# Kernel optimization log

Measured on AMD Instinct MI355X. Metric: run time of the kernel, lower is better.

The kernel has to match this reference:

```python
import jax, jax.numpy as jnp
import numpy as np
import math

B, S, D, H = 16, 1024, 1024, 16
HD = D // H  # head_dim = 64

def setup_inputs() -> dict:
    key = jax.random.key(0)
    ks = jax.random.split(key, 10)
    def lin_w(k, out_d, in_d):
        bound = 1.0 / math.sqrt(in_d)
        return jax.random.uniform(k, (out_d, in_d), jnp.float32, -bound, bound)
    return {
        "x": jax.random.normal(ks[0], (B, S, D), jnp.float32),
        "attention_mask_indices": jnp.ones((B, S, 1), dtype=bool),
        "wq_w": lin_w(ks[1], D, D), "wq_b": jnp.zeros((D,), jnp.float32),
        "wk_w": lin_w(ks[2], D, D), "wk_b": jnp.zeros((D,), jnp.float32),
        "wv_w": lin_w(ks[3], D, D), "wv_b": jnp.zeros((D,), jnp.float32),
        "wo_w": lin_w(ks[4], D, D), "wo_b": jnp.zeros((D,), jnp.float32),
    }

def reference(x, attention_mask_indices, wq_w, wq_b, wk_w, wk_b, wv_w, wv_b, wo_w, wo_b):
    bsz, seqlen, _ = x.shape
    # torch Linear: y = x @ W^T + b
    xq = (x @ wq_w.T + wq_b).reshape(bsz, seqlen, H, HD)
    xk = (x @ wk_w.T + wk_b).reshape(bsz, seqlen, H, HD)
    xv = (x @ wv_w.T + wv_b).reshape(bsz, seqlen, H, HD)
    # n_kv_heads == n_heads -> repeat_kv is identity
    scores = jnp.einsum("bqhd,bkhd->bhqk", xq, xk) / math.sqrt(HD)
    mask = attention_mask_indices[:, None, None, :, 0]  # [b,1,1,s]
    scores = jnp.where(mask, scores, jnp.finfo(scores.dtype).min)
    probs = jax.nn.softmax(scores.astype(jnp.float32), axis=-1)
    out = jnp.einsum("bhqk,bkhd->bqhd", probs, xv).reshape(bsz, seqlen, D)
    return out @ wo_w.T + wo_b
```

## Files before the change

kernel.cpp:

```cpp
#include <hip/hip_runtime.h>
#include <hip/hip_bf16.h>

typedef __bf16 bf16;
typedef bf16  bf16x4 __attribute__((ext_vector_type(4)));
typedef bf16  bf16x8 __attribute__((ext_vector_type(8)));
typedef float f32x4  __attribute__((ext_vector_type(4)));

#define B_  16
#define S_  1024
#define D_  1024
#define H_  16
#define HD_ 64

typedef __attribute__((address_space(3))) void lds_void_t;
typedef __attribute__((address_space(1))) void g_void_t;
__device__ __forceinline__ void gl_lds16(const void* g, void* l) {
    __builtin_amdgcn_global_load_lds(
        (const g_void_t*)(uintptr_t)g,
        (lds_void_t*)(uint32_t)(uintptr_t)l, 16, 0, 0);
}

#define BARRIER()     asm volatile("s_barrier" ::: "memory")
#define WAIT_LGKM(n)  do { asm volatile("s_waitcnt lgkmcnt(" #n ")" ::: "memory"); \
                           __builtin_amdgcn_sched_barrier(0); } while (0)
#define WAIT_VM(n)    asm volatile("s_waitcnt vmcnt(" #n ")" ::: "memory")
#define SCHED_PIN()   __builtin_amdgcn_sched_barrier(0)
#define PRIO1()       __builtin_amdgcn_s_setprio(1)
#define PRIO0()       __builtin_amdgcn_s_setprio(0)

__global__ __launch_bounds__(256) void cvt_f32_bf16(
    const float* __restrict__ s, bf16* __restrict__ d, int n)
{
    int i = (blockIdx.x * 256 + threadIdx.x) * 8;
    if (i >= n) return;
    f32x4 a = *(const f32x4*)(s + i);
    f32x4 b = *(const f32x4*)(s + i + 4);
    bf16x8 r;
    for (int j = 0; j < 4; j++) { r[j] = (bf16)a[j]; r[4 + j] = (bf16)b[j]; }
    *(bf16x8*)(d + i) = r;
}

template <bool QKV, int NBY, typename TC>
__global__ __launch_bounds__(512, 2) void gemm8(
    const bf16* __restrict__ A, const bf16* __restrict__ Bw,
    const float* __restrict__ b0, const float* __restrict__ b1,
    const float* __restrict__ b2,
    TC* __restrict__ C, int ldc,
    bf16* __restrict__ Qd, bf16* __restrict__ Kd, bf16* __restrict__ Vd)
{
    __shared__ char lds[131072];

    const int tid  = threadIdx.x;
    const int w    = tid >> 6;
    const int lane = tid & 63;
    const int l15  = lane & 15;
    const int quad = lane >> 4;
    const int wm   = w >> 2;
    const int wn   = w & 3;

    const int nwg = gridDim.x;
    const int lin = blockIdx.x;
    const int swz = (lin & 7) * (nwg >> 3) + (lin >> 3);
    const int bx  = swz / NBY;
    const int by  = swz - bx * NBY;
    const int m0  = bx * 256;
    const int n0  = by * 256;

    const int rl0 = w * 16 + (lane >> 3);
    const int rl1 = rl0 + 8;
    const int sc  = (((lane & 7) ^ ((lane >> 3) & 7))) * 16;
    char* const ld0 = (char*)lds + w * 2048;

    const char* aS0; const char* aS1;
    int bidx = 0, m0loc = 0;
    if constexpr (QKV) {
        aS0 = (const char*)A + (size_t)(m0 + rl0) * 2048 + sc;
        aS1 = (const char*)A + (size_t)(m0 + rl1) * 2048 + sc;
    } else {
        bidx  = m0 >> 10; m0loc = m0 & 1023;
        aS0 = (const char*)A + ((size_t)bidx * 16 * 1024 + m0loc + rl0) * 128 + sc;
        aS1 = (const char*)A + ((size_t)bidx * 16 * 1024 + m0loc + rl1) * 128 + sc;
    }
    const char* bS0 = (const char*)Bw + (size_t)(n0 + rl0) * 2048 + sc;
    const char* bS1 = (const char*)Bw + (size_t)(n0 + rl1) * 2048 + sc;

    auto stageA = [&](int slot, int t, int half) {
        size_t go;
        if constexpr (QKV) go = (size_t)half * 262144 + (size_t)t * 128;
        else               go = (size_t)t * 131072 + (size_t)half * 16384;
        gl_lds16(aS0 + go, ld0 + slot * 16384);
        gl_lds16(aS1 + go, ld0 + slot * 16384 + 1024);
    };
    auto stageB = [&](int slot, int t, int half) {
        size_t go = (size_t)half * 262144 + (size_t)t * 128;
        gl_lds16(bS0 + go, ld0 + slot * 16384);
        gl_lds16(bS1 + go, ld0 + slot * 16384 + 1024);
    };

    const int cx0 = ((quad    ) ^ (l15 & 7)) * 16;
    const int cx1 = ((quad | 4) ^ (l15 & 7)) * 16;
    const char* aEv0 = (char*)lds + wm * 16384 + l15 * 128 + cx0;
    const char* aEv1 = (char*)lds + wm * 16384 + l15 * 128 + cx1;
    const char* bEv0 = (char*)lds + 32768 + (wn >> 1) * 16384 + (wn & 1) * 8192
                       + l15 * 128 + cx0;
    const char* bEv1 = (char*)lds + 32768 + (wn >> 1) * 16384 + (wn & 1) * 8192
                       + l15 * 128 + cx1;
    const char* aOd0 = aEv0 + 65536;
    const char* aOd1 = aEv1 + 65536;
    const char* bOd0 = bEv0 + 65536;
    const char* bOd1 = bEv1 + 65536;

    bf16x8 a03[4][2], a47[4][2], bE[4][2], bO[4][2];
    f32x4 acc[8][4];
    #pragma unroll
    for (int i = 0; i < 8; i++)
        #pragma unroll
        for (int j = 0; j < 4; j++)
            acc[i][j] = (f32x4){0.f, 0.f, 0.f, 0.f};

    auto rdA = [&](bf16x8 (&dst)[4][2], const char* p0, const char* p1, int ro) {
        #pragma unroll
        for (int mf = 0; mf < 4; mf++) {
            dst[mf][0] = *(const bf16x8*)(p0 + (ro + mf) * 2048);
            dst[mf][1] = *(const bf16x8*)(p1 + (ro + mf) * 2048);
        }
    };
    auto rdB2 = [&](bf16x8 (&dst)[4][2], int lo, const char* p0, const char* p1) {
        #pragma unroll
        for (int nf = 0; nf < 2; nf++) {
            dst[lo + nf][0] = *(const bf16x8*)(p0 + (lo + nf) * 2048);
            dst[lo + nf][1] = *(const bf16x8*)(p1 + (lo + nf) * 2048);
        }
    };
    auto mfq = [&](bf16x8 (&af)[4][2], bf16x8 (&bf_)[4][2], int nlo, int mlo) {
        #pragma unroll
        for (int mf = 0; mf < 4; mf++)
            #pragma unroll
            for (int nf = 0; nf < 2; nf++) {
                f32x4 c = acc[mlo + mf][nlo + nf];
                c = __builtin_amdgcn_mfma_f32_16x16x32_bf16(
                        af[mf][0], bf_[nlo + nf][0], c, 0, 0, 0);
                c = __builtin_amdgcn_mfma_f32_16x16x32_bf16(
                        af[mf][1], bf_[nlo + nf][1], c, 0, 0, 0);
                acc[mlo + mf][nlo + nf] = c;
            }
    };

    stageA(0, 0, 0); stageA(1, 0, 1); stageB(2, 0, 0); stageB(3, 0, 1);
    stageB(6, 1, 0); stageB(7, 1, 1);
    stageA(4, 1, 0); stageA(5, 1, 1);
    WAIT_VM(8);
    BARRIER();
    rdA(a03, aEv0, aEv1, 0);

    for (int i = 0; i < 8; ++i) {
        const int t2 = (2 * i + 2) & 15, t3 = (2 * i + 3) & 15;
        rdB2(bE, 0, bEv0, bEv1);
        WAIT_LGKM(0); PRIO1(); mfq(a03, bE, 0, 0); PRIO0(); BARRIER();
        rdB2(bE, 2, bEv0, bEv1);
        SCHED_PIN();
        rdA(a47, aEv0, aEv1, 4);
        WAIT_LGKM(8); PRIO1(); mfq(a03, bE, 2, 0); PRIO0();
        WAIT_VM(0); BARRIER();
        rdA(a03, aOd0, aOd1, 0);
        stageB(2, t2, 0); stageB(3, t2, 1);
        WAIT_LGKM(8); PRIO1(); mfq(a47, bE, 0, 4); PRIO0(); BARRIER();
        rdB2(bO, 0, bOd0, bOd1);
        stageA(0, t2, 0); stageA(1, t2, 1);
        WAIT_LGKM(8); PRIO1(); mfq(a47, bE, 2, 4); PRIO0(); BARRIER();
        rdB2(bO, 2, bOd0, bOd1);
        SCHED_PIN();
        rdA(a47, aOd0, aOd1, 4);
        WAIT_LGKM(8); PRIO1(); mfq(a03, bO, 0, 0); PRIO0(); BARRIER();
        stageB(6, t3, 0);
        WAIT_LGKM(8); PRIO1(); mfq(a03, bO, 2, 0); PRIO0();
        WAIT_VM(2); BARRIER();
        rdA(a03, aEv0, aEv1, 0);
        stageB(7, t3, 1);
        WAIT_LGKM(8); PRIO1(); mfq(a47, bO, 0, 4); PRIO0(); BARRIER();
        stageA(4, t3, 0); stageA(5, t3, 1);
        WAIT_LGKM(8); PRIO1(); mfq(a47, bO, 2, 4); PRIO0();
        WAIT_VM(4); BARRIER();
    }

    if constexpr (QKV) {
        const int seg = n0 >> 10;
        const int cb  = n0 & 1023;
        const float* bp = seg == 0 ? b0 : (seg == 1 ? b1 : b2);
        if (seg < 2) {
            bf16* dst = (seg == 0) ? Qd : Kd;
            #pragma unroll
            for (int mf = 0; mf < 8; mf++)
                #pragma unroll
                for (int nf = 0; nf < 4; nf++) {
                    int col = cb + wn * 64 + nf * 16 + l15;
                    int hh = col >> 6, dd = col & 63;
                    float bb = bp[col];
                    #pragma unroll
                    for (int r = 0; r < 4; r++) {
                        int row = m0 + wm * 128 + mf * 16 + quad * 4 + r;
                        int bl = row >> 10, s = row & 1023;
                        dst[((size_t)(bl * 16 + hh) * 1024 + s) * 64 + dd] =
                            (bf16)(acc[mf][nf][r] + bb);
                    }
                }
        } else {
            #pragma unroll
            for (int mf = 0; mf < 8; mf++)
                #pragma unroll
                for (int nf = 0; nf < 4; nf++) {
                    int col = cb + wn * 64 + nf * 16 + l15;
                    int hh = col >> 6, dd = col & 63;
                    float bb = bp[col];
                    int row0 = m0 + wm * 128 + mf * 16 + quad * 4;
                    int bl = row0 >> 10, s0 = row0 & 1023;
                    bf16x4 pk;
                    #pragma unroll
                    for (int r = 0; r < 4; r++) pk[r] = (bf16)(acc[mf][nf][r] + bb);
                    *(bf16x4*)&Vd[(((size_t)(bl * 16 + hh) * 16 + (s0 >> 6)) * 64 + dd) * 64
                                  + (s0 & 63)] = pk;
                }
        }
    } else {
        #pragma unroll
        for (int mf = 0; mf < 8; mf++)
            #pragma unroll
            for (int nf = 0; nf < 4; nf++) {
                int col = n0 + wn * 64 + nf * 16 + l15;
                float bb = b0[col];
                #pragma unroll
                for (int r = 0; r < 4; r++) {
                    int row = m0 + wm * 128 + mf * 16 + quad * 4 + r;
                    C[(size_t)row * ldc + col] = (TC)(acc[mf][nf][r] + bb);
                }
            }
    }
}

__global__ __launch_bounds__(256) void attn_fused(
    bf16* __restrict__ Qh, const bf16* __restrict__ Kh,
    const bf16* __restrict__ Vt)
{
    const int qt = blockIdx.x, h = blockIdx.y, b = blockIdx.z;
    const int tid  = threadIdx.x;
    const int w    = tid >> 6;
    const int lane = tid & 63;
    const int l15  = lane & 15;
    const int quad = lane >> 4;

    __shared__ bf16 lds[36864];
    bf16* Pw = lds + 18432 + w * 4608;

    const int nIss = (w == 0) ? 3 : 2;
    int gofs[3];
    for (int j = 0; j < nIss; j++) {
        int c = (w + j * 4) * 64 + lane;
        int row = c / 9;
        int o = c - row * 9;
        if (o == 8) o = 0;
        gofs[j] = (row * 8 + o) * 16;
    }

    const float qscale = 0.125f * 1.44269504088896f;
    bf16* Qbase = Qh + ((size_t)(b * 16 + h) * 1024 + qt * 256 + w * 64) * 64;
    bf16x8 aq[4][2];
    for (int mt = 0; mt < 4; mt++)
        for (int c = 0; c < 2; c++) {
            bf16x8 v = *(const bf16x8*)&Qbase[(mt * 16 + l15) * 64 + c * 32 + quad * 8];
            for (int j = 0; j < 8; j++) v[j] = (bf16)((float)v[j] * qscale);
            aq[mt][c] = v;
        }

    bf16x8 ones;
    for (int j = 0; j < 8; j++) ones[j] = (bf16)1.0f;

    f32x4 acc[4][4], accL[4];
    for (int i = 0; i < 4; i++) {
        accL[i] = (f32x4){0.f, 0.f, 0.f, 0.f};
        for (int j = 0; j < 4; j++) acc[i][j] = (f32x4){0.f, 0.f, 0.f, 0.f};
    }

    const bf16* Ktb = Kh + (size_t)(b * 16 + h) * 65536;
    const bf16* Vtb = Vt + (size_t)(b * 16 + h) * 65536;

    auto stage = [&](int kt, int cur) {
        const char* Ktile = (const char*)(Ktb + kt * 4096);
        const char* Vtile = (const char*)(Vtb + kt * 4096);
        char* Kd = (char*)lds + cur * 18432;
        for (int j = 0; j < nIss; j++) {
            int is = w + j * 4;
            gl_lds16(Ktile + gofs[j], Kd + is * 1024);
            gl_lds16(Vtile + gofs[j], Kd + 9216 + is * 1024);
        }
    };

    stage(0, 0);

    for (int kt = 0; kt < 16; kt++) {
        const int cur = kt & 1;
        if (kt < 15) {
            stage(kt + 1, cur ^ 1);
            if (w == 0) { WAIT_VM(6); } else { WAIT_VM(4); }
        } else {
            WAIT_VM(0);
        }
        BARRIER();

        const bf16* Ks = lds + cur * 9216;
        const bf16* Vs = Ks + 4608;

        bf16x8 bk[4][2];
        for (int nt = 0; nt < 4; nt++)
            for (int c = 0; c < 2; c++)
                bk[nt][c] = *(const bf16x8*)&Ks[(nt * 16 + l15) * 72 + c * 32 + quad * 8];

        f32x4 sf[4][4];
        for (int nt = 0; nt < 4; nt++)
            for (int mt = 0; mt < 4; mt++) {
                f32x4 z = (f32x4){0.f, 0.f, 0.f, 0.f};
                z = __builtin_amdgcn_mfma_f32_16x16x32_bf16(bk[nt][0], aq[mt][0], z, 0, 0, 0);
                sf[nt][mt] = __builtin_amdgcn_mfma_f32_16x16x32_bf16(bk[nt][1], aq[mt][1], z, 0, 0, 0);
            }

        for (int mt = 0; mt < 4; mt++)
            for (int nt = 0; nt < 4; nt++) {
                bf16x4 pk;
                for (int r = 0; r < 4; r++)
                    pk[r] = (bf16)__builtin_amdgcn_exp2f(sf[nt][mt][r]);
                *(bf16x4*)&Pw[(mt * 16 + l15) * 72 + nt * 16 + quad * 4] = pk;
            }

        WAIT_LGKM(0);

        bf16x8 pa[4][2];
        for (int mt = 0; mt < 4; mt++)
            for (int c = 0; c < 2; c++)
                pa[mt][c] = *(const bf16x8*)&Pw[(mt * 16 + l15) * 72 + c * 32 + quad * 8];
        for (int mt = 0; mt < 4; mt++) {
            accL[mt] = __builtin_amdgcn_mfma_f32_16x16x32_bf16(pa[mt][0], ones, accL[mt], 0, 0, 0);
            accL[mt] = __builtin_amdgcn_mfma_f32_16x16x32_bf16(pa[mt][1], ones, accL[mt], 0, 0, 0);
        }
        bf16x8 bv[4][2];
        for (int nt = 0; nt < 4; nt++)
            for (int c = 0; c < 2; c++)
                bv[nt][c] = *(const bf16x8*)&Vs[(nt * 16 + l15) * 72 + c * 32 + quad * 8];
        for (int mt = 0; mt < 4; mt++)
            for (int nt = 0; nt < 4; nt++) {
                acc[mt][nt] = __builtin_amdgcn_mfma_f32_16x16x32_bf16(pa[mt][0], bv[nt][0], acc[mt][nt], 0, 0, 0);
                acc[mt][nt] = __builtin_amdgcn_mfma_f32_16x16x32_bf16(pa[mt][1], bv[nt][1], acc[mt][nt], 0, 0, 0);
            }
        BARRIER();
    }

    for (int mt = 0; mt < 4; mt++)
        for (int r = 0; r < 4; r++) {
            float rl = 1.f / accL[mt][r];
            for (int nt = 0; nt < 4; nt++)
                Qbase[(mt * 16 + quad * 4 + r) * 64 + nt * 16 + l15] =
                    (bf16)(acc[mt][nt][r] * rl);
        }
}

extern "C" void kernel_launch(void* const* d_in, const int* in_sizes, int n_in,
                              void* d_out, int out_size, void* d_ws, size_t ws_size,
                              hipStream_t stream)
{
    const float* x    = (const float*)d_in[0];
    const float* wq_w = (const float*)d_in[2];
    const float* wq_b = (const float*)d_in[3];
    const float* wk_w = (const float*)d_in[4];
    const float* wk_b = (const float*)d_in[5];
    const float* wv_w = (const float*)d_in[6];
    const float* wv_b = (const float*)d_in[7];
    const float* wo_w = (const float*)d_in[8];
    const float* wo_b = (const float*)d_in[9];
    float* out = (float*)d_out;

    const size_t MEL = 1024 * 1024;
    int CH = 16;
    if (ws_size != 0)
        while (CH > 1 && (4 + 4 * (size_t)CH) * MEL * sizeof(bf16) > ws_size) CH >>= 1;

    bf16* wqkvb = (bf16*)d_ws;
    bf16* wob   = wqkvb + 3 * MEL;
    bf16* xb    = wob + MEL;
    bf16* Qh    = xb + (size_t)CH * MEL;
    bf16* Kh    = Qh + (size_t)CH * MEL;
    bf16* Vtb   = Kh + (size_t)CH * MEL;

    dim3 blk(256);
    cvt_f32_bf16<<<512, blk, 0, stream>>>(wq_w, wqkvb,           (int)MEL);
    cvt_f32_bf16<<<512, blk, 0, stream>>>(wk_w, wqkvb + MEL,     (int)MEL);
    cvt_f32_bf16<<<512, blk, 0, stream>>>(wv_w, wqkvb + 2 * MEL, (int)MEL);
    cvt_f32_bf16<<<512, blk, 0, stream>>>(wo_w, wob,             (int)MEL);

    for (int c0 = 0; c0 < B_; c0 += CH) {
        const int Mc = CH * S_;
        cvt_f32_bf16<<<Mc * 1024 / 2048, blk, 0, stream>>>(
            x + (size_t)c0 * S_ * D_, xb, Mc * 1024);

        gemm8<true, 12, bf16><<<dim3((Mc / 256) * 12), dim3(512), 0, stream>>>(
            xb, wqkvb, wq_b, wk_b, wv_b,
            (bf16*)nullptr, 0, Qh, Kh, Vtb);

        attn_fused<<<dim3(4, H_, CH), blk, 0, stream>>>(Qh, Kh, Vtb);

        gemm8<false, 4, float><<<dim3((Mc / 256) * 4), dim3(512), 0, stream>>>(
            Qh, wob, wo_b, nullptr, nullptr,
            out + (size_t)c0 * S_ * D_, 1024, nullptr, nullptr, nullptr);
    }
}
```

Before: 396.1 us.

## Pass attention probabilities through registers via bpermute and drop P LDS buffer

Replaces the per-wave LDS round trip for the softmax probability tile with ds_bpermute lane shuffles that rearrange the S-MFMA output into the A-operand layout for the PV MFMA. The row sum moves from extra MFMAs against a ones vector to scalar accumulation plus cross-lane shuffles at the end. This halves the shared memory footprint, sets launch bounds to ask for 3 blocks per CU, and remaps block indices so neighbouring blocks are spread across batch-heads. The aim is fewer LDS writes and reads, less MFMA work and higher occupancy, at the cost of more VALU and bpermute traffic and possible register pressure.

```diff
diff --git a/kernel.cpp b/kernel.cpp
--- a/kernel.cpp
+++ b/kernel.cpp
@@ -237,19 +237,22 @@
     }
 }
 
-__global__ __launch_bounds__(256) void attn_fused(
+__global__ __launch_bounds__(256, 3) void attn_fused(
     bf16* __restrict__ Qh, const bf16* __restrict__ Kh,
     const bf16* __restrict__ Vt)
 {
-    const int qt = blockIdx.x, h = blockIdx.y, b = blockIdx.z;
     const int tid  = threadIdx.x;
     const int w    = tid >> 6;
     const int lane = tid & 63;
     const int l15  = lane & 15;
     const int quad = lane >> 4;
 
-    __shared__ bf16 lds[36864];
-    bf16* Pw = lds + 18432 + w * 4608;
+    const int lin = blockIdx.x + (blockIdx.y << 2) + (blockIdx.z << 6);
+    const int ppx = (int)gridDim.z * 2;
+    const int bh  = (lin & 7) * ppx + ((lin >> 3) >> 2);
+    const int qt  = (lin >> 3) & 3;
+
+    __shared__ bf16 lds[18432];
 
     const int nIss = (w == 0) ? 3 : 2;
     int gofs[3];
@@ -262,26 +265,27 @@
     }
 
     const float qscale = 0.125f * 1.44269504088896f;
-    bf16* Qbase = Qh + ((size_t)(b * 16 + h) * 1024 + qt * 256 + w * 64) * 64;
+    bf16* Qbase = Qh + ((size_t)bh * 1024 + qt * 256 + w * 64) * 64;
     bf16x8 aq[4][2];
+    #pragma unroll
     for (int mt = 0; mt < 4; mt++)
+        #pragma unroll
         for (int c = 0; c < 2; c++) {
             bf16x8 v = *(const bf16x8*)&Qbase[(mt * 16 + l15) * 64 + c * 32 + quad * 8];
+            #pragma unroll
             for (int j = 0; j < 8; j++) v[j] = (bf16)((float)v[j] * qscale);
             aq[mt][c] = v;
         }
 
-    bf16x8 ones;
-    for (int j = 0; j < 8; j++) ones[j] = (bf16)1.0f;
-
-    f32x4 acc[4][4], accL[4];
-    for (int i = 0; i < 4; i++) {
-        accL[i] = (f32x4){0.f, 0.f, 0.f, 0.f};
+    f32x4 acc[4][4];
+    float lsum[4] = {0.f, 0.f, 0.f, 0.f};
+    #pragma unroll
+    for (int i = 0; i < 4; i++)
+        #pragma unroll
         for (int j = 0; j < 4; j++) acc[i][j] = (f32x4){0.f, 0.f, 0.f, 0.f};
-    }
-
-    const bf16* Ktb = Kh + (size_t)(b * 16 + h) * 65536;
-    const bf16* Vtb = Vt + (size_t)(b * 16 + h) * 65536;
+
+    const bf16* Ktb = Kh + (size_t)bh * 65536;
+    const bf16* Vtb = Vt + (size_t)bh * 65536;
 
     auto stage = [&](int kt, int cur) {
         const char* Ktile = (const char*)(Ktb + kt * 4096);
@@ -294,6 +298,11 @@
         }
     };
 
+    const bool qe = ((quad & 1) == 0);
+    const bool ql = (quad < 2);
+    const int  a1 = (l15 + 16 * (((quad & 1) << 1) | (quad >> 1))) << 2;
+    const int  a2 = a1 ^ 64;
+
     stage(0, 0);
 
     for (int kt = 0; kt < 16; kt++) {
@@ -309,52 +318,82 @@
         const bf16* Ks = lds + cur * 9216;
         const bf16* Vs = Ks + 4608;
 
-        bf16x8 bk[4][2];
-        for (int nt = 0; nt < 4; nt++)
-            for (int c = 0; c < 2; c++)
-                bk[nt][c] = *(const bf16x8*)&Ks[(nt * 16 + l15) * 72 + c * 32 + quad * 8];
-
-        f32x4 sf[4][4];
-        for (int nt = 0; nt < 4; nt++)
+        #pragma unroll
+        for (int c = 0; c < 2; c++) {
+            bf16x8 bkt[2][2], bvc[4];
+            #pragma unroll
+            for (int t = 0; t < 2; t++)
+                #pragma unroll
+                for (int cd = 0; cd < 2; cd++)
+                    bkt[t][cd] = *(const bf16x8*)
+                        &Ks[((2 * c + t) * 16 + l15) * 72 + cd * 32 + quad * 8];
+            #pragma unroll
+            for (int nt = 0; nt < 4; nt++)
+                bvc[nt] = *(const bf16x8*)&Vs[(nt * 16 + l15) * 72 + c * 32 + quad * 8];
+
+            f32x4 sf2[2][4];
+            #pragma unroll
+            for (int t = 0; t < 2; t++)
+                #pragma unroll
+                for (int mt = 0; mt < 4; mt++) {
+                    f32x4 z = (f32x4){0.f, 0.f, 0.f, 0.f};
+                    z = __builtin_amdgcn_mfma_f32_16x16x32_bf16(bkt[t][0], aq[mt][0], z, 0, 0, 0);
+                    sf2[t][mt] = __builtin_amdgcn_mfma_f32_16x16x32_bf16(bkt[t][1], aq[mt][1], z, 0, 0, 0);
+                }
+
+            unsigned lo2[2][4], hi2[2][4];
+            #pragma unroll
+            for (int t = 0; t < 2; t++)
+                #pragma unroll
+                for (int mt = 0; mt < 4; mt++) {
+                    bf16 h0 = (bf16)__builtin_amdgcn_exp2f(sf2[t][mt][0]);
+                    bf16 h1 = (bf16)__builtin_amdgcn_exp2f(sf2[t][mt][1]);
+                    bf16 h2 = (bf16)__builtin_amdgcn_exp2f(sf2[t][mt][2]);
+                    bf16 h3 = (bf16)__builtin_amdgcn_exp2f(sf2[t][mt][3]);
+                    lsum[mt] += ((float)h0 + (float)h1) + ((float)h2 + (float)h3);
+                    union { bf16 h[2]; unsigned u; } p0, p1;
+                    p0.h[0] = h0; p0.h[1] = h1;
+                    p1.h[0] = h2; p1.h[1] = h3;
+                    lo2[t][mt] = p0.u;
+                    hi2[t][mt] = p1.u;
+                }
+
+            #pragma unroll
             for (int mt = 0; mt < 4; mt++) {
-                f32x4 z = (f32x4){0.f, 0.f, 0.f, 0.f};
-                z = __builtin_amdgcn_mfma_f32_16x16x32_bf16(bk[nt][0], aq[mt][0], z, 0, 0, 0);
-                sf[nt][mt] = __builtin_amdgcn_mfma_f32_16x16x32_bf16(bk[nt][1], aq[mt][1], z, 0, 0, 0);
+                unsigned aLo = lo2[0][mt], aHi = hi2[0][mt];
+                unsigned bLo = lo2[1][mt], bHi = hi2[1][mt];
+                int g1 = __builtin_amdgcn_ds_bpermute(a1, (int)(qe ? aLo : bLo));
+                int g2 = __builtin_amdgcn_ds_bpermute(a1, (int)(qe ? aHi : bHi));
+                int g3 = __builtin_amdgcn_ds_bpermute(a2, (int)(qe ? bLo : aLo));
+                int g4 = __builtin_amdgcn_ds_bpermute(a2, (int)(qe ? bHi : aHi));
+                union { unsigned u[4]; bf16x8 v; } pw;
+                pw.u[0] = (unsigned)(ql ? g1 : g3);
+                pw.u[1] = (unsigned)(ql ? g2 : g4);
+                pw.u[2] = (unsigned)(ql ? g3 : g1);
+                pw.u[3] = (unsigned)(ql ? g4 : g2);
+                #pragma unroll
+                for (int nt = 0; nt < 4; nt++)
+                    acc[mt][nt] = __builtin_amdgcn_mfma_f32_16x16x32_bf16(
+                        pw.v, bvc[nt], acc[mt][nt], 0, 0, 0);
             }
-
-        for (int mt = 0; mt < 4; mt++)
-            for (int nt = 0; nt < 4; nt++) {
-                bf16x4 pk;
-                for (int r = 0; r < 4; r++)
-                    pk[r] = (bf16)__builtin_amdgcn_exp2f(sf[nt][mt][r]);
-                *(bf16x4*)&Pw[(mt * 16 + l15) * 72 + nt * 16 + quad * 4] = pk;
-            }
-
-        WAIT_LGKM(0);
-
-        bf16x8 pa[4][2];
-        for (int mt = 0; mt < 4; mt++)
-            for (int c = 0; c < 2; c++)
-                pa[mt][c] = *(const bf16x8*)&Pw[(mt * 16 + l15) * 72 + c * 32 + quad * 8];
-        for (int mt = 0; mt < 4; mt++) {
-            accL[mt] = __builtin_amdgcn_mfma_f32_16x16x32_bf16(pa[mt][0], ones, accL[mt], 0, 0, 0);
-            accL[mt] = __builtin_amdgcn_mfma_f32_16x16x32_bf16(pa[mt][1], ones, accL[mt], 0, 0, 0);
-        }
-        bf16x8 bv[4][2];
-        for (int nt = 0; nt < 4; nt++)
-            for (int c = 0; c < 2; c++)
-                bv[nt][c] = *(const bf16x8*)&Vs[(nt * 16 + l15) * 72 + c * 32 + quad * 8];
-        for (int mt = 0; mt < 4; mt++)
-            for (int nt = 0; nt < 4; nt++) {
-                acc[mt][nt] = __builtin_amdgcn_mfma_f32_16x16x32_bf16(pa[mt][0], bv[nt][0], acc[mt][nt], 0, 0, 0);
-                acc[mt][nt] = __builtin_amdgcn_mfma_f32_16x16x32_bf16(pa[mt][1], bv[nt][1], acc[mt][nt], 0, 0, 0);
-            }
+        }
         BARRIER();
     }
 
+    float lf[4];
+    #pragma unroll
+    for (int mt = 0; mt < 4; mt++) {
+        float v = lsum[mt];
+        v += __shfl_xor(v, 16);
+        v += __shfl_xor(v, 32);
+        lf[mt] = v;
+    }
+    #pragma unroll
     for (int mt = 0; mt < 4; mt++)
+        #pragma unroll
         for (int r = 0; r < 4; r++) {
-            float rl = 1.f / accL[mt][r];
+            float rl = 1.f / __shfl(lf[mt], quad * 4 + r);
+            #pragma unroll
             for (int nt = 0; nt < 4; nt++)
                 Qbase[(mt * 16 + quad * 4 + r) * 64 + nt * 16 + l15] =
                     (bf16)(acc[mt][nt][r] * rl);
```

After: 588.0 us. 48.5% more time.
